# Kernel tuning notes

Measured on AMD Instinct MI355X. Metric: run time of the kernel, lower is better.

Reference implementation:

```python
import jax, jax.numpy as jnp
import numpy as np

B, L = 2048, 200
D_MODEL, HIDDEN, V = 512, 256, 40000
LN_EPS = 1e-5


def setup_inputs() -> dict:
    key = jax.random.key(0)
    ks = jax.random.split(key, 10)
    return {
        "hidden": jax.random.normal(ks[0], (B, D_MODEL), dtype=jnp.float32),
        "loc_seq": jax.random.randint(ks[1], (B, L), 0, V, dtype=jnp.int32),
        "mask": jax.random.randint(ks[2], (B, L), 0, 2, dtype=jnp.int32),
        # learned_head params
        "W1": jax.random.normal(ks[3], (D_MODEL, HIDDEN), dtype=jnp.float32) / np.sqrt(D_MODEL),
        "b1": jnp.zeros((HIDDEN,), dtype=jnp.float32),
        "gamma": jnp.ones((HIDDEN,), dtype=jnp.float32),
        "beta": jnp.zeros((HIDDEN,), dtype=jnp.float32),
        "W2": jax.random.normal(ks[4], (HIDDEN, V), dtype=jnp.float32) / np.sqrt(HIDDEN),
        "b2": jnp.zeros((V,), dtype=jnp.float32),
        # scalar weights (match torch init values)
        "recency_weight": jnp.asarray(3.0, dtype=jnp.float32),
        "frequency_weight": jnp.asarray(2.0, dtype=jnp.float32),
        "history_scale": jnp.asarray(8.0, dtype=jnp.float32),
        "learned_scale": jnp.asarray(0.5, dtype=jnp.float32),
    }


def _history_scores(loc_seq, mask, recency_weight, frequency_weight, history_scale):
    # Per-(b,t) contribution: recency term exp(-0.1*(L-1-t))*recency_weight
    # plus frequency term frequency_weight per valid occurrence.
    Lcur = loc_seq.shape[1]
    t = jnp.arange(Lcur, dtype=jnp.float32)
    recency = jnp.exp(-0.1 * (Lcur - 1.0 - t)) * recency_weight  # (L,)
    maskf = mask.astype(jnp.float32)                              # (B,L)
    vals = (recency[None, :] + frequency_weight) * maskf          # (B,L)
    Bcur = loc_seq.shape[0]
    b_idx = jnp.arange(Bcur)[:, None]                             # (B,1)
    scores = jnp.zeros((Bcur, V), dtype=jnp.float32).at[b_idx, loc_seq].add(vals)
    return scores * history_scale


def reference(hidden, loc_seq, mask, W1, b1, gamma, beta, W2, b2,
              recency_weight, frequency_weight, history_scale, learned_scale):
    # learned head: Linear -> LayerNorm -> GELU -> (Dropout inactive in eval) -> Linear
    h = hidden @ W1 + b1                                          # (B,HIDDEN)
    mu = jnp.mean(h, axis=-1, keepdims=True)
    var = jnp.mean(jnp.square(h - mu), axis=-1, keepdims=True)
    h = (h - mu) * jax.lax.rsqrt(var + LN_EPS) * gamma + beta
    h = jax.nn.gelu(h, approximate=False)
    learned_logits = h @ W2 + b2                                  # (B,V)
    hist = _history_scores(loc_seq, mask, recency_weight, frequency_weight, history_scale)
    return learned_logits * learned_scale + hist
```

## Files before the change

kernel.cpp:

```cpp
#include <hip/hip_runtime.h>
#include <hip/hip_bf16.h>

#define B_   2048
#define L_   200
#define DM_  512
#define HID_ 256
#define V_   40000
#define NPAD 40064
#define LN_EPS 1e-5f

typedef short bf16x8 __attribute__((ext_vector_type(8)));
typedef float f32x4  __attribute__((ext_vector_type(4)));

#define GLOAD_LDS16(g, l)                                                     \
    __builtin_amdgcn_global_load_lds(                                         \
        (const __attribute__((address_space(1))) void*)(g),                   \
        (__attribute__((address_space(3))) void*)(l), 16, 0, 0)

__global__ __launch_bounds__(256) void transpose_w2(const float* __restrict__ W2,
                                                    __hip_bfloat16* __restrict__ WT) {
    __shared__ float tile[64][65];
    const int n0 = blockIdx.x * 64;
    const int k0 = blockIdx.y * 64;
    const int tid = threadIdx.x;

    const int c = tid & 63, r4 = tid >> 6;
#pragma unroll
    for (int p = 0; p < 16; ++p) {
        int r = p * 4 + r4;
        int n = n0 + c;
        tile[r][c] = (n < V_) ? W2[(size_t)(k0 + r) * V_ + n] : 0.f;
    }
    __syncthreads();

    const int kl = (tid & 31) * 2, nl4 = tid >> 5;
#pragma unroll
    for (int p = 0; p < 8; ++p) {
        int nl = p * 8 + nl4;
        __hip_bfloat162 h2;
        h2.x = __float2bfloat16(tile[kl][nl]);
        h2.y = __float2bfloat16(tile[kl + 1][nl]);
        *(__hip_bfloat162*)(WT + (size_t)(n0 + nl) * HID_ + k0 + kl) = h2;
    }
}

__global__ __launch_bounds__(256) void head_kernel(const float* __restrict__ hidden,
                                                   const float* __restrict__ W1,
                                                   const float* __restrict__ b1,
                                                   const float* __restrict__ gamma,
                                                   const float* __restrict__ beta,
                                                   __hip_bfloat16* __restrict__ hout) {
    __shared__ float hid[8][DM_];
    __shared__ float red[2][8][4];
    const int r0 = blockIdx.x * 8;
    const int tid = threadIdx.x;

    {
        const float4* src = (const float4*)(hidden + (size_t)r0 * DM_);
        float4* dst = (float4*)(&hid[0][0]);
        for (int i = tid; i < 8 * DM_ / 4; i += 256) dst[i] = src[i];
    }
    __syncthreads();

    float acc[8] = {0.f, 0.f, 0.f, 0.f, 0.f, 0.f, 0.f, 0.f};
#pragma unroll 4
    for (int k = 0; k < DM_; ++k) {
        float w = W1[(size_t)k * HID_ + tid];
#pragma unroll
        for (int r = 0; r < 8; ++r) acc[r] = fmaf(hid[r][k], w, acc[r]);
    }

    const float b1v = b1[tid], gv = gamma[tid], bev = beta[tid];
    const int lane = tid & 63, wv = tid >> 6;

#pragma unroll
    for (int r = 0; r < 8; ++r) {
        float v = acc[r] + b1v;
        float s = v, q = v * v;
#pragma unroll
        for (int off = 1; off < 64; off <<= 1) {
            s += __shfl_xor(s, off);
            q += __shfl_xor(q, off);
        }
        if (lane == 0) { red[0][r][wv] = s; red[1][r][wv] = q; }
    }
    __syncthreads();

#pragma unroll
    for (int r = 0; r < 8; ++r) {
        float s  = red[0][r][0] + red[0][r][1] + red[0][r][2] + red[0][r][3];
        float q  = red[1][r][0] + red[1][r][1] + red[1][r][2] + red[1][r][3];
        float mu = s * (1.f / HID_);
        float var = q * (1.f / HID_) - mu * mu;
        float v  = acc[r] + b1v;
        float hn = (v - mu) * rsqrtf(var + LN_EPS) * gv + bev;
        float g  = 0.5f * hn * (1.f + erff(hn * 0.70710678118654752f));
        hout[(size_t)(r0 + r) * HID_ + tid] = __float2bfloat16(g);
    }
}

#define BM 128
#define BN 128
#define BK 64

__global__ __launch_bounds__(256) void gemm_kernel(const __hip_bfloat16* __restrict__ hA,
                                                   const __hip_bfloat16* __restrict__ BT,
                                                   const float* __restrict__ b2,
                                                   const float* __restrict__ lsp,
                                                   float* __restrict__ out) {
    __shared__ __hip_bfloat16 As[BM * BK];
    __shared__ __hip_bfloat16 Bs[BN * BK];

    const int r0 = blockIdx.x * BM;
    const int c0 = blockIdx.y * BN;
    const int tid = threadIdx.x;
    const int lane = tid & 63;
    const int wv = tid >> 6;
    const int wr = (wv >> 1) * 64;
    const int wc = (wv & 1) * 64;
    const float ls = lsp[0];

    f32x4 acc[4][4];
#pragma unroll
    for (int m = 0; m < 4; ++m)
#pragma unroll
        for (int n = 0; n < 4; ++n) acc[m][n] = (f32x4){0.f, 0.f, 0.f, 0.f};

    const int rsub = lane >> 3;
    const int kswz = (((lane & 7) ^ rsub) << 3);
    const __hip_bfloat16* aBase = hA + (size_t)r0 * HID_;
    const __hip_bfloat16* bBase = BT + (size_t)c0 * HID_;

    for (int kk = 0; kk < HID_; kk += BK) {
#pragma unroll
        for (int i = 0; i < 4; ++i) {
            int ch  = wv * 4 + i;
            int row = ch * 8 + rsub;
            GLOAD_LDS16(aBase + (size_t)row * HID_ + kk + kswz,
                        (char*)As + ch * 1024);
            GLOAD_LDS16(bBase + (size_t)row * HID_ + kk + kswz,
                        (char*)Bs + ch * 1024);
        }
        __syncthreads();

#pragma unroll
        for (int ks = 0; ks < BK / 32; ++ks) {
            const int kb = ks * 32 + ((lane >> 4) << 3);
            const int ke = kb ^ ((lane & 7) << 3);
            bf16x8 af[4], bf[4];
            const int rb = wr + (lane & 15);
            const int cb = wc + (lane & 15);
#pragma unroll
            for (int m = 0; m < 4; ++m)
                af[m] = *(const bf16x8*)(As + (rb + m * 16) * BK + ke);
#pragma unroll
            for (int n = 0; n < 4; ++n)
                bf[n] = *(const bf16x8*)(Bs + (cb + n * 16) * BK + ke);
#pragma unroll
            for (int m = 0; m < 4; ++m)
#pragma unroll
                for (int n = 0; n < 4; ++n)
                    acc[m][n] = __builtin_amdgcn_mfma_f32_16x16x32_bf16(
                        af[m], bf[n], acc[m][n], 0, 0, 0);
        }
        __syncthreads();
    }

    const int colb = c0 + wc + (lane & 15);
    const int rowb = r0 + wr + ((lane >> 4) << 2);
    float b2v[4];
#pragma unroll
    for (int n = 0; n < 4; ++n) {
        int col = colb + n * 16;
        b2v[n] = (col < V_) ? b2[col] : 0.f;
    }
#pragma unroll
    for (int m = 0; m < 4; ++m) {
        float* orow = out + (size_t)(rowb + m * 16) * V_;
#pragma unroll
        for (int n = 0; n < 4; ++n) {
            int col = colb + n * 16;
            if (col < V_) {
#pragma unroll
                for (int j = 0; j < 4; ++j)
                    orow[(size_t)j * V_ + col] = (acc[m][n][j] + b2v[n]) * ls;
            }
        }
    }
}

__global__ __launch_bounds__(256) void hist_kernel(const int* __restrict__ loc,
                                                   const int* __restrict__ mask,
                                                   const float* __restrict__ rw,
                                                   const float* __restrict__ fw,
                                                   const float* __restrict__ hs,
                                                   float* __restrict__ out) {
    const int idx = blockIdx.x * 256 + threadIdx.x;
    if (idx >= B_ * L_) return;
    const int b = idx / L_, t = idx - b * L_;
    if (mask[idx] != 0) {
        float recency = expf(-0.1f * (float)(L_ - 1 - t)) * rw[0];
        float val = (recency + fw[0]) * hs[0];
        atomicAdd(out + (size_t)b * V_ + loc[idx], val);
    }
}

extern "C" void kernel_launch(void* const* d_in, const int* in_sizes, int n_in,
                              void* d_out, int out_size, void* d_ws, size_t ws_size,
                              hipStream_t stream) {
    const float* hidden = (const float*)d_in[0];
    const int*   loc    = (const int*)d_in[1];
    const int*   mask   = (const int*)d_in[2];
    const float* W1     = (const float*)d_in[3];
    const float* b1     = (const float*)d_in[4];
    const float* gamma  = (const float*)d_in[5];
    const float* beta   = (const float*)d_in[6];
    const float* W2     = (const float*)d_in[7];
    const float* b2     = (const float*)d_in[8];
    const float* rw     = (const float*)d_in[9];
    const float* fw     = (const float*)d_in[10];
    const float* hs     = (const float*)d_in[11];
    const float* ls     = (const float*)d_in[12];
    float* out = (float*)d_out;

    __hip_bfloat16* WT   = (__hip_bfloat16*)d_ws;
    __hip_bfloat16* hbuf = (__hip_bfloat16*)((char*)d_ws + 20512768);

    transpose_w2<<<dim3(NPAD / 64, HID_ / 64), 256, 0, stream>>>(W2, WT);
    head_kernel<<<B_ / 8, 256, 0, stream>>>(hidden, W1, b1, gamma, beta, hbuf);
    gemm_kernel<<<dim3(B_ / BM, NPAD / BN), 256, 0, stream>>>(hbuf, WT, b2, ls, out);
    hist_kernel<<<(B_ * L_ + 255) / 256, 256, 0, stream>>>(loc, mask, rw, fw, hs, out);
}
```

Before: 204.4 us.

## Vectorize output stores, double-buffer GEMM, split-K head and wider transpose stores

The MFMA operands are swapped so each lane holds four consecutive output columns, which allows float4 stores of the large logits tensor and float4 loads of b2. The GEMM K loop is double-buffered in LDS so the next tile's global-to-LDS loads overlap compute. The head kernel now uses 512 threads that split K in two and combine partial sums through LDS. The W2 transpose writes 16-byte bf16 vectors. The risks are a __syncthreads inside a branch taken only by half the head-kernel threads, and higher LDS use per GEMM block.

```diff
diff --git a/kernel.cpp b/kernel.cpp
--- a/kernel.cpp
+++ b/kernel.cpp
@@ -33,83 +33,96 @@
     }
     __syncthreads();
 
-    const int kl = (tid & 31) * 2, nl4 = tid >> 5;
-#pragma unroll
-    for (int p = 0; p < 8; ++p) {
-        int nl = p * 8 + nl4;
-        __hip_bfloat162 h2;
-        h2.x = __float2bfloat16(tile[kl][nl]);
-        h2.y = __float2bfloat16(tile[kl + 1][nl]);
-        *(__hip_bfloat162*)(WT + (size_t)(n0 + nl) * HID_ + k0 + kl) = h2;
-    }
-}
-
-__global__ __launch_bounds__(256) void head_kernel(const float* __restrict__ hidden,
+    const int nl = tid >> 3;
+    const int kb = (tid & 7) * 8;
+#pragma unroll
+    for (int p = 0; p < 2; ++p) {
+        int n = p * 32 + nl;
+        bf16x8 v;
+#pragma unroll
+        for (int j = 0; j < 8; ++j) {
+            __hip_bfloat16 h = __float2bfloat16(tile[kb + j][n]);
+            v[j] = *(short*)&h;
+        }
+        *(bf16x8*)(WT + (size_t)(n0 + n) * HID_ + k0 + kb) = v;
+    }
+}
+
+__global__ __launch_bounds__(512) void head_kernel(const float* __restrict__ hidden,
                                                    const float* __restrict__ W1,
                                                    const float* __restrict__ b1,
                                                    const float* __restrict__ gamma,
                                                    const float* __restrict__ beta,
                                                    __hip_bfloat16* __restrict__ hout) {
     __shared__ float hid[8][DM_];
+    __shared__ float part[8][HID_];
     __shared__ float red[2][8][4];
     const int r0 = blockIdx.x * 8;
     const int tid = threadIdx.x;
+    const int col = tid & 255, half = tid >> 8;
 
     {
         const float4* src = (const float4*)(hidden + (size_t)r0 * DM_);
         float4* dst = (float4*)(&hid[0][0]);
-        for (int i = tid; i < 8 * DM_ / 4; i += 256) dst[i] = src[i];
+        for (int i = tid; i < 8 * DM_ / 4; i += 512) dst[i] = src[i];
     }
     __syncthreads();
 
     float acc[8] = {0.f, 0.f, 0.f, 0.f, 0.f, 0.f, 0.f, 0.f};
-#pragma unroll 4
-    for (int k = 0; k < DM_; ++k) {
-        float w = W1[(size_t)k * HID_ + tid];
+    const int kbeg = half * (DM_ / 2);
+#pragma unroll 8
+    for (int k = kbeg; k < kbeg + DM_ / 2; ++k) {
+        float w = W1[(size_t)k * HID_ + col];
 #pragma unroll
         for (int r = 0; r < 8; ++r) acc[r] = fmaf(hid[r][k], w, acc[r]);
     }
 
-    const float b1v = b1[tid], gv = gamma[tid], bev = beta[tid];
-    const int lane = tid & 63, wv = tid >> 6;
-
-#pragma unroll
-    for (int r = 0; r < 8; ++r) {
-        float v = acc[r] + b1v;
-        float s = v, q = v * v;
-#pragma unroll
-        for (int off = 1; off < 64; off <<= 1) {
-            s += __shfl_xor(s, off);
-            q += __shfl_xor(q, off);
-        }
-        if (lane == 0) { red[0][r][wv] = s; red[1][r][wv] = q; }
-    }
-    __syncthreads();
-
-#pragma unroll
-    for (int r = 0; r < 8; ++r) {
-        float s  = red[0][r][0] + red[0][r][1] + red[0][r][2] + red[0][r][3];
-        float q  = red[1][r][0] + red[1][r][1] + red[1][r][2] + red[1][r][3];
-        float mu = s * (1.f / HID_);
-        float var = q * (1.f / HID_) - mu * mu;
-        float v  = acc[r] + b1v;
-        float hn = (v - mu) * rsqrtf(var + LN_EPS) * gv + bev;
-        float g  = 0.5f * hn * (1.f + erff(hn * 0.70710678118654752f));
-        hout[(size_t)(r0 + r) * HID_ + tid] = __float2bfloat16(g);
+    if (half == 1) {
+#pragma unroll
+        for (int r = 0; r < 8; ++r) part[r][col] = acc[r];
+    }
+    __syncthreads();
+    if (half == 0) {
+        const float b1v = b1[col], gv = gamma[col], bev = beta[col];
+        const int lane = col & 63, wv = col >> 6;
+        float v[8];
+#pragma unroll
+        for (int r = 0; r < 8; ++r) {
+            v[r] = acc[r] + part[r][col] + b1v;
+            float s = v[r], q = v[r] * v[r];
+#pragma unroll
+            for (int off = 1; off < 64; off <<= 1) {
+                s += __shfl_xor(s, off);
+                q += __shfl_xor(q, off);
+            }
+            if (lane == 0) { red[0][r][wv] = s; red[1][r][wv] = q; }
+        }
+        __syncthreads();
+#pragma unroll
+        for (int r = 0; r < 8; ++r) {
+            float s  = red[0][r][0] + red[0][r][1] + red[0][r][2] + red[0][r][3];
+            float q  = red[1][r][0] + red[1][r][1] + red[1][r][2] + red[1][r][3];
+            float mu = s * (1.f / HID_);
+            float var = q * (1.f / HID_) - mu * mu;
+            float hn = (v[r] - mu) * rsqrtf(var + LN_EPS) * gv + bev;
+            float g  = 0.5f * hn * (1.f + erff(hn * 0.70710678118654752f));
+            hout[(size_t)(r0 + r) * HID_ + col] = __float2bfloat16(g);
+        }
     }
 }
 
 #define BM 128
 #define BN 128
 #define BK 64
-
-__global__ __launch_bounds__(256) void gemm_kernel(const __hip_bfloat16* __restrict__ hA,
-                                                   const __hip_bfloat16* __restrict__ BT,
-                                                   const float* __restrict__ b2,
-                                                   const float* __restrict__ lsp,
-                                                   float* __restrict__ out) {
-    __shared__ __hip_bfloat16 As[BM * BK];
-    __shared__ __hip_bfloat16 Bs[BN * BK];
+#define NT (HID_ / BK)
+
+__global__ __launch_bounds__(256, 2) void gemm_kernel(const __hip_bfloat16* __restrict__ hA,
+                                                      const __hip_bfloat16* __restrict__ BT,
+                                                      const float* __restrict__ b2,
+                                                      const float* __restrict__ lsp,
+                                                      float* __restrict__ out) {
+    __shared__ __hip_bfloat16 As[2][BM * BK];
+    __shared__ __hip_bfloat16 Bs[2][BN * BK];
 
     const int r0 = blockIdx.x * BM;
     const int c0 = blockIdx.y * BN;
@@ -128,20 +141,29 @@
 
     const int rsub = lane >> 3;
     const int kswz = (((lane & 7) ^ rsub) << 3);
-    const __hip_bfloat16* aBase = hA + (size_t)r0 * HID_;
-    const __hip_bfloat16* bBase = BT + (size_t)c0 * HID_;
-
-    for (int kk = 0; kk < HID_; kk += BK) {
-#pragma unroll
-        for (int i = 0; i < 4; ++i) {
-            int ch  = wv * 4 + i;
-            int row = ch * 8 + rsub;
-            GLOAD_LDS16(aBase + (size_t)row * HID_ + kk + kswz,
-                        (char*)As + ch * 1024);
-            GLOAD_LDS16(bBase + (size_t)row * HID_ + kk + kswz,
-                        (char*)Bs + ch * 1024);
-        }
-        __syncthreads();
+    const __hip_bfloat16* aB = hA + (size_t)r0 * HID_;
+    const __hip_bfloat16* bB = BT + (size_t)c0 * HID_;
+
+#define STAGE(buf, kk)                                                        \
+    {                                                                         \
+        _Pragma("unroll")                                                     \
+        for (int i = 0; i < 4; ++i) {                                         \
+            int ch  = wv * 4 + i;                                             \
+            int row = ch * 8 + rsub;                                          \
+            GLOAD_LDS16(aB + (size_t)row * HID_ + (kk) + kswz,                \
+                        (char*)As[buf] + ch * 1024);                          \
+            GLOAD_LDS16(bB + (size_t)row * HID_ + (kk) + kswz,                \
+                        (char*)Bs[buf] + ch * 1024);                          \
+        }                                                                     \
+    }
+
+    STAGE(0, 0);
+    __syncthreads();
+
+#pragma unroll
+    for (int t = 0; t < NT; ++t) {
+        const int cur = t & 1;
+        if (t + 1 < NT) STAGE(cur ^ 1, (t + 1) * BK);
 
 #pragma unroll
         for (int ks = 0; ks < BK / 32; ++ks) {
@@ -152,41 +174,46 @@
             const int cb = wc + (lane & 15);
 #pragma unroll
             for (int m = 0; m < 4; ++m)
-                af[m] = *(const bf16x8*)(As + (rb + m * 16) * BK + ke);
+                af[m] = *(const bf16x8*)(As[cur] + (rb + m * 16) * BK + ke);
 #pragma unroll
             for (int n = 0; n < 4; ++n)
-                bf[n] = *(const bf16x8*)(Bs + (cb + n * 16) * BK + ke);
+                bf[n] = *(const bf16x8*)(Bs[cur] + (cb + n * 16) * BK + ke);
 #pragma unroll
             for (int m = 0; m < 4; ++m)
 #pragma unroll
                 for (int n = 0; n < 4; ++n)
                     acc[m][n] = __builtin_amdgcn_mfma_f32_16x16x32_bf16(
-                        af[m], bf[n], acc[m][n], 0, 0, 0);
+                        bf[n], af[m], acc[m][n], 0, 0, 0);
         }
         __syncthreads();
     }
 
-    const int colb = c0 + wc + (lane & 15);
-    const int rowb = r0 + wr + ((lane >> 4) << 2);
-    float b2v[4];
+    const int orow = r0 + wr + (lane & 15);
+    const int ocol = c0 + wc + ((lane >> 4) << 2);
+    float4 b2v[4];
 #pragma unroll
     for (int n = 0; n < 4; ++n) {
-        int col = colb + n * 16;
-        b2v[n] = (col < V_) ? b2[col] : 0.f;
+        int col = ocol + n * 16;
+        b2v[n] = (col < V_) ? *(const float4*)(b2 + col)
+                            : (float4){0.f, 0.f, 0.f, 0.f};
     }
 #pragma unroll
     for (int m = 0; m < 4; ++m) {
-        float* orow = out + (size_t)(rowb + m * 16) * V_;
+        float* orp = out + (size_t)(orow + m * 16) * V_;
 #pragma unroll
         for (int n = 0; n < 4; ++n) {
-            int col = colb + n * 16;
+            int col = ocol + n * 16;
             if (col < V_) {
-#pragma unroll
-                for (int j = 0; j < 4; ++j)
-                    orow[(size_t)j * V_ + col] = (acc[m][n][j] + b2v[n]) * ls;
+                float4 o;
+                o.x = (acc[m][n][0] + b2v[n].x) * ls;
+                o.y = (acc[m][n][1] + b2v[n].y) * ls;
+                o.z = (acc[m][n][2] + b2v[n].z) * ls;
+                o.w = (acc[m][n][3] + b2v[n].w) * ls;
+                *(float4*)(orp + col) = o;
             }
         }
     }
+#undef STAGE
 }
 
 __global__ __launch_bounds__(256) void hist_kernel(const int* __restrict__ loc,
@@ -227,7 +254,7 @@
     __hip_bfloat16* hbuf = (__hip_bfloat16*)((char*)d_ws + 20512768);
 
     transpose_w2<<<dim3(NPAD / 64, HID_ / 64), 256, 0, stream>>>(W2, WT);
-    head_kernel<<<B_ / 8, 256, 0, stream>>>(hidden, W1, b1, gamma, beta, hbuf);
+    head_kernel<<<B_ / 8, 512, 0, stream>>>(hidden, W1, b1, gamma, beta, hbuf);
     gemm_kernel<<<dim3(B_ / BM, NPAD / BN), 256, 0, stream>>>(hbuf, WT, b2, ls, out);
     hist_kernel<<<(B_ * L_ + 255) / 256, 256, 0, stream>>>(loc, mask, rw, fw, hs, out);
 }
```

After: 198.2 us. 3.0% less time.
